# Kernel optimization log

Hardware: AMD Instinct MI355X
Metric: run time of the kernel (lower is better)

## Reference

```python
import jax, jax.numpy as jnp
import numpy as np

CENTER_VAR = 0.1
SIZE_VAR = 0.2
EPS = 1e-8


def setup_inputs() -> dict:
    key = jax.random.key(0)
    k1, k2, k3, k4, k5, k6 = jax.random.split(key, 6)
    B, P, C = 8, 2048, 21
    confidence = jax.random.normal(k1, (B, P, C), dtype=jnp.float32)
    locations = jax.random.normal(k2, (B, P, 4), dtype=jnp.float32)
    target_confidence = jax.random.randint(k3, (B, P), 0, 2).astype(jnp.int64)
    target_locations = jax.random.normal(k4, (B, P, 4), dtype=jnp.float32)
    # priors in center-offset form (cx, cy, w, h), valid positive sizes
    cxcy = jax.random.uniform(k5, (P, 2), jnp.float32, 0.05, 0.95)
    wh = jax.random.uniform(k6, (P, 2), jnp.float32, 0.02, 0.3)
    priors = jnp.concatenate([cxcy, wh], axis=-1)
    return {"confidence": confidence, "locations": locations,
            "target_confidence": target_confidence,
            "target_locations": target_locations, "priors": priors}


def _decode(loc, priors):
    # loc: [B,P,4], priors: [P,4] center form -> corner-form boxes [B,P,4]
    cxcy = priors[None, :, 0:2] + loc[:, :, 0:2] * CENTER_VAR * priors[None, :, 2:4]
    wh = priors[None, :, 2:4] * jnp.exp(loc[:, :, 2:4] * SIZE_VAR)
    mn = cxcy - wh * 0.5
    return jnp.concatenate([mn, mn + wh], axis=-1)


def _giou_pair(a, b):
    # a: [A,4], b: [B,4] corner form -> pairwise GIoU [A,B]
    inter_mx = jnp.minimum(a[:, None, 2:4], b[None, :, 2:4])
    inter_mn = jnp.maximum(a[:, None, 0:2], b[None, :, 0:2])
    inter = jnp.prod(jnp.clip(inter_mx - inter_mn, 0.0, None), axis=-1)
    area_a = ((a[:, 2] - a[:, 0]) * (a[:, 3] - a[:, 1]))[:, None]
    area_b = ((b[:, 2] - b[:, 0]) * (b[:, 3] - b[:, 1]))[None, :]
    union = area_a + area_b - inter
    iou = inter / jnp.maximum(union, EPS)
    enc_mx = jnp.maximum(a[:, None, 2:4], b[None, :, 2:4])
    enc_mn = jnp.minimum(a[:, None, 0:2], b[None, :, 0:2])
    enc = jnp.prod(enc_mx - enc_mn, axis=-1)
    return iou - (enc - union) / jnp.maximum(enc, EPS)


def reference(confidence, locations, target_confidence, target_locations, priors):
    probs = jax.nn.softmax(confidence, axis=-1)
    max_p = probs.max(axis=-1)
    max_i = probs.argmax(axis=-1)
    pos_target = target_confidence > 0                       # [B,P]
    pos_infer = pos_target & (max_p > 0.5) & (max_i > 0)     # [B,P]
    dec_loc = _decode(locations, priors)                     # [B,P,4]
    dec_tgt = _decode(target_locations, priors)              # [B,P,4]

    def per_batch(dl, dt, mi, mt):
        g = _giou_pair(dl, dt)                               # [P,P]
        pair_mask = mi[:, None] & mt[None, :]
        s = jnp.sum(jnp.where(pair_mask, g, 0.0))
        nt = jnp.sum(mt).astype(jnp.float32)
        na = jnp.sum(mi).astype(jnp.float32)
        both = (nt > 0) & (na > 0)
        one = (nt > 0) ^ (na > 0)
        # sum_b[pos_t] (1 - sum_a[pos_i] giou[a,b] / nt) = nt - s/nt
        term = jnp.where(both, nt - s / jnp.maximum(nt, 1.0),
                         jnp.where(one, 1.0, 0.0))
        return term, nt

    terms, nts = jax.vmap(per_batch)(dec_loc, dec_tgt, pos_infer, pos_target)
    num_boxes = jnp.sum(nts)
    return jnp.sum(terms) / jnp.maximum(num_boxes, 1.0)
```

## Files before the change

kernel.cpp:

```cpp
#include <hip/hip_runtime.h>

#define EPSV 1e-8f
#define CENTER_VAR 0.1f
#define SIZE_VAR 0.2f
#define WSZ 64
#define MAXA 2048

__device__ __forceinline__ float4 decode_box(float4 loc, float4 pr) {
    float cx = pr.x + loc.x * CENTER_VAR * pr.z;
    float cy = pr.y + loc.y * CENTER_VAR * pr.w;
    float w  = pr.z * __expf(loc.z * SIZE_VAR);
    float h  = pr.w * __expf(loc.w * SIZE_VAR);
    float x0 = cx - w * 0.5f;
    float y0 = cy - h * 0.5f;
    return make_float4(x0, y0, x0 + w, y0 + h);
}

__device__ __forceinline__ float giou_pair(float4 A, float4 Bx) {
    float ix = fminf(A.z, Bx.z) - fmaxf(A.x, Bx.x);
    float iy = fminf(A.w, Bx.w) - fmaxf(A.y, Bx.y);
    float inter = fmaxf(ix, 0.f) * fmaxf(iy, 0.f);
    float area_a = (A.z - A.x) * (A.w - A.y);
    float area_b = (Bx.z - Bx.x) * (Bx.w - Bx.y);
    float uni = area_a + area_b - inter;
    float iou = __fdividef(inter, fmaxf(uni, EPSV));
    float ex = fmaxf(A.z, Bx.z) - fminf(A.x, Bx.x);
    float ey = fmaxf(A.w, Bx.w) - fminf(A.y, Bx.y);
    float enc = ex * ey;
    return iou - __fdividef(enc - uni, fmaxf(enc, EPSV));
}

__global__ __launch_bounds__(WSZ) void mask_kernel(
    const float* __restrict__ conf,
    const float* __restrict__ loc,
    const int*   __restrict__ tconf,
    const float* __restrict__ priors,
    int P, int C, int bpb,
    int* __restrict__ done,
    int* __restrict__ cnt_a, int* __restrict__ cnt_t,
    float4* __restrict__ regions) {
    int blk = blockIdx.x;
    int lane = threadIdx.x;
    int b = blk / bpb;
    int p = (blk - b * bpb) * WSZ + lane;
    size_t idx = (size_t)b * P + p;
    bool live = p < P;

    if (blk == 0 && lane == 0) *done = 0;

    bool pos_t = live && (tconf[idx] > 0);
    unsigned long long bm_t = __ballot(pos_t);

    bool inf = false;
    float4 box = make_float4(0.f, 0.f, 0.f, 0.f);
    if (pos_t) {
        const float* cf = conf + idx * C;
        float m; int mi; float se;
        if (C == 21) {
            float v[21];
            #pragma unroll
            for (int c = 0; c < 21; ++c) v[c] = cf[c];
            m = v[0]; mi = 0;
            #pragma unroll
            for (int c = 1; c < 21; ++c) { if (v[c] > m) { m = v[c]; mi = c; } }
            se = 0.f;
            #pragma unroll
            for (int c = 0; c < 21; ++c) se += __expf(v[c] - m);
        } else {
            m = cf[0]; mi = 0;
            for (int c = 1; c < C; ++c) { float v = cf[c]; if (v > m) { m = v; mi = c; } }
            se = 0.f;
            for (int c = 0; c < C; ++c) se += __expf(cf[c] - m);
        }
        if (se < 2.0f && mi > 0) {
            float4 l  = ((const float4*)loc)[idx];
            float4 pr = ((const float4*)priors)[p];
            box = decode_box(l, pr);
            inf = true;
        }
    }
    unsigned long long bm_i = __ballot(inf);
    if (inf) {
        int k = __popcll(bm_i & ((1ull << lane) - 1ull));
        regions[(size_t)blk * WSZ + k] = box;
    }
    if (lane == 0) {
        cnt_t[blk] = __popcll(bm_t);
        cnt_a[blk] = __popcll(bm_i);
    }
}

__global__ __launch_bounds__(WSZ) void pair_kernel(
    const int*   __restrict__ tconf,
    const float* __restrict__ tloc,
    const float* __restrict__ priors,
    const float4* __restrict__ regions,
    const int* __restrict__ cnt_a, const int* __restrict__ cnt_t,
    int* __restrict__ done,
    float* __restrict__ s_part,
    int B, int P, int bpb, int nblk,
    float* __restrict__ out) {
    int blk = blockIdx.x;
    int lane = threadIdx.x;
    int b = blk / bpb;
    int base = b * bpb;
    int p = (blk - base) * WSZ + lane;
    size_t idx = (size_t)b * P + p;
    bool live = p < P;

    __shared__ float4 ab[MAXA];
    __shared__ int cnts[64];

    cnts[lane] = (lane < bpb) ? cnt_a[base + lane] : 0;
    __syncthreads();
    int nA = 0;
    for (int r = 0; r < bpb; ++r) {
        int c = cnts[r];
        for (int i = lane; i < c; i += WSZ)
            ab[nA + i] = regions[(size_t)(base + r) * WSZ + i];
        nA += c;
    }
    __syncthreads();

    bool pos_t = live && (tconf[idx] > 0);
    float acc = 0.f;
    if (pos_t && nA > 0) {
        float4 l  = ((const float4*)tloc)[idx];
        float4 pr = ((const float4*)priors)[p];
        float4 T = decode_box(l, pr);
        for (int i = 0; i < nA; ++i) acc += giou_pair(ab[i], T);
    }
    for (int off = 32; off > 0; off >>= 1) acc += __shfl_down(acc, off);
    if (lane == 0) s_part[blk] = acc;
    __threadfence();

    int last = 0;
    if (lane == 0) {
        int old = __hip_atomic_fetch_add(done, 1, __ATOMIC_ACQ_REL,
                                         __HIP_MEMORY_SCOPE_AGENT);
        last = (old == nblk - 1);
    }
    last = __shfl(last, 0);
    if (!last) return;

    __shared__ float sb[16];
    __shared__ int   ntb[16], nab[16];
    if (lane < 16) { sb[lane] = 0.f; ntb[lane] = 0; nab[lane] = 0; }
    __syncthreads();
    for (int slot = lane; slot < nblk; slot += WSZ) {
        int bb = slot / bpb;
        float sv = __hip_atomic_load(&s_part[slot], __ATOMIC_RELAXED,
                                     __HIP_MEMORY_SCOPE_AGENT);
        atomicAdd(&sb[bb], sv);
        atomicAdd(&ntb[bb], cnt_t[slot]);
        atomicAdd(&nab[bb], cnt_a[slot]);
    }
    __syncthreads();
    if (lane == 0) {
        float tsum = 0.f, nsum = 0.f;
        for (int bb = 0; bb < B; ++bb) {
            float ntf = (float)ntb[bb];
            bool bt = ntb[bb] > 0, ba = nab[bb] > 0;
            float term = (bt && ba) ? (ntf - sb[bb] / fmaxf(ntf, 1.f))
                                    : ((bt != ba) ? 1.f : 0.f);
            tsum += term;
            nsum += ntf;
        }
        out[0] = tsum / fmaxf(nsum, 1.f);
    }
}

extern "C" void kernel_launch(void* const* d_in, const int* in_sizes, int n_in,
                              void* d_out, int out_size, void* d_ws, size_t ws_size,
                              hipStream_t stream) {
    const float* conf   = (const float*)d_in[0];
    const float* loc    = (const float*)d_in[1];
    const int*   tconf  = (const int*)  d_in[2];
    const float* tloc   = (const float*)d_in[3];
    const float* priors = (const float*)d_in[4];
    float* out = (float*)d_out;

    int P = in_sizes[4] / 4;
    int B = in_sizes[2] / P;
    int C = in_sizes[0] / (B * P);
    int bpb  = (P + WSZ - 1) / WSZ;
    int nblk = B * bpb;

    int*   done   = (int*)d_ws;
    int*   cnt_a  = done + 4;
    int*   cnt_t  = cnt_a + nblk;
    float* s_part = (float*)(cnt_t + nblk);
    size_t hdr = (16 + (size_t)nblk * 3 * sizeof(int) + 15) & ~(size_t)15;
    float4* regions = (float4*)((char*)d_ws + hdr);

    mask_kernel<<<nblk, WSZ, 0, stream>>>(conf, loc, tconf, priors,
                                          P, C, bpb, done, cnt_a, cnt_t, regions);
    pair_kernel<<<nblk, WSZ, 0, stream>>>(tconf, tloc, priors, regions,
                                          cnt_a, cnt_t, done, s_part,
                                          B, P, bpb, nblk, out);
}
```

Before: 83.82 us.

## Use 256-thread blocks, ballot bitmasks and a separate finalize kernel

Raises blocks from one 64-lane wave to four waves. This cuts the number of blocks that each copy a batch's candidate boxes into shared memory. The mask kernel now stores per-wave ballot bitmasks, so the pair kernel no longer reloads target_confidence. The last-block atomic counter with its thread fence is replaced by a third single-block kernel that does the final reduction. The trade-offs are one extra kernel launch, fewer blocks in flight on a large GPU, and the removal of bounds checks, so P must be a multiple of 256.

```diff
diff --git a/kernel.cpp b/kernel.cpp
--- a/kernel.cpp
+++ b/kernel.cpp
@@ -3,7 +3,7 @@
 #define EPSV 1e-8f
 #define CENTER_VAR 0.1f
 #define SIZE_VAR 0.2f
-#define WSZ 64
+#define TPB 256
 #define MAXA 2048
 
 __device__ __forceinline__ float4 decode_box(float4 loc, float4 pr) {
@@ -30,31 +30,28 @@
     return iou - __fdividef(enc - uni, fmaxf(enc, EPSV));
 }
 
-__global__ __launch_bounds__(WSZ) void mask_kernel(
+__global__ __launch_bounds__(TPB) void mask_kernel(
     const float* __restrict__ conf,
     const float* __restrict__ loc,
     const int*   __restrict__ tconf,
     const float* __restrict__ priors,
-    int P, int C, int bpb,
-    int* __restrict__ done,
-    int* __restrict__ cnt_a, int* __restrict__ cnt_t,
+    int P, int C,
+    int* __restrict__ cnt_a,
+    unsigned long long* __restrict__ masks,
     float4* __restrict__ regions) {
-    int blk = blockIdx.x;
-    int lane = threadIdx.x;
-    int b = blk / bpb;
-    int p = (blk - b * bpb) * WSZ + lane;
-    size_t idx = (size_t)b * P + p;
-    bool live = p < P;
-
-    if (blk == 0 && lane == 0) *done = 0;
-
-    bool pos_t = live && (tconf[idx] > 0);
+    int g = blockIdx.x * TPB + threadIdx.x;
+    int lane = threadIdx.x & 63;
+    int b = g / P;
+    int p = g - b * P;
+    int ws = g >> 6;
+
+    bool pos_t = tconf[g] > 0;
     unsigned long long bm_t = __ballot(pos_t);
 
     bool inf = false;
-    float4 box = make_float4(0.f, 0.f, 0.f, 0.f);
+    float4 box;
     if (pos_t) {
-        const float* cf = conf + idx * C;
+        const float* cf = conf + (size_t)g * C;
         float m; int mi; float se;
         if (C == 21) {
             float v[21];
@@ -73,7 +70,7 @@
             for (int c = 0; c < C; ++c) se += __expf(cf[c] - m);
         }
         if (se < 2.0f && mi > 0) {
-            float4 l  = ((const float4*)loc)[idx];
+            float4 l  = ((const float4*)loc)[g];
             float4 pr = ((const float4*)priors)[p];
             box = decode_box(l, pr);
             inf = true;
@@ -82,81 +79,91 @@
     unsigned long long bm_i = __ballot(inf);
     if (inf) {
         int k = __popcll(bm_i & ((1ull << lane) - 1ull));
-        regions[(size_t)blk * WSZ + k] = box;
+        regions[((size_t)ws << 6) + k] = box;
     }
     if (lane == 0) {
-        cnt_t[blk] = __popcll(bm_t);
-        cnt_a[blk] = __popcll(bm_i);
-    }
-}
-
-__global__ __launch_bounds__(WSZ) void pair_kernel(
-    const int*   __restrict__ tconf,
+        masks[ws] = bm_t;
+        cnt_a[ws] = __popcll(bm_i);
+    }
+}
+
+__global__ __launch_bounds__(TPB) void pair_kernel(
     const float* __restrict__ tloc,
     const float* __restrict__ priors,
     const float4* __restrict__ regions,
-    const int* __restrict__ cnt_a, const int* __restrict__ cnt_t,
-    int* __restrict__ done,
+    const int* __restrict__ cnt_a,
+    const unsigned long long* __restrict__ masks,
     float* __restrict__ s_part,
-    int B, int P, int bpb, int nblk,
-    float* __restrict__ out) {
+    int P) {
     int blk = blockIdx.x;
-    int lane = threadIdx.x;
-    int b = blk / bpb;
-    int base = b * bpb;
-    int p = (blk - base) * WSZ + lane;
-    size_t idx = (size_t)b * P + p;
-    bool live = p < P;
+    int g = blk * TPB + threadIdx.x;
+    int lane = threadIdx.x & 63, wid = threadIdx.x >> 6;
+    int b = g / P;
+    int p = g - b * P;
+    int ws = g >> 6;
+    int wpb = P >> 6;
+    int base_ws = b * wpb;
 
     __shared__ float4 ab[MAXA];
     __shared__ int cnts[64];
-
-    cnts[lane] = (lane < bpb) ? cnt_a[base + lane] : 0;
+    __shared__ float wsum[TPB / 64];
+
+    for (int i = threadIdx.x; i < wpb; i += TPB) cnts[i] = cnt_a[base_ws + i];
     __syncthreads();
     int nA = 0;
-    for (int r = 0; r < bpb; ++r) {
+    for (int r = 0; r < wpb; ++r) {
         int c = cnts[r];
-        for (int i = lane; i < c; i += WSZ)
-            ab[nA + i] = regions[(size_t)(base + r) * WSZ + i];
+        for (int i = threadIdx.x; i < c; i += TPB)
+            ab[nA + i] = regions[((size_t)(base_ws + r) << 6) + i];
         nA += c;
     }
     __syncthreads();
 
-    bool pos_t = live && (tconf[idx] > 0);
+    unsigned long long bm = masks[ws];
+    bool pos_t = (bm >> lane) & 1ull;
     float acc = 0.f;
     if (pos_t && nA > 0) {
-        float4 l  = ((const float4*)tloc)[idx];
+        float4 l  = ((const float4*)tloc)[g];
         float4 pr = ((const float4*)priors)[p];
         float4 T = decode_box(l, pr);
         for (int i = 0; i < nA; ++i) acc += giou_pair(ab[i], T);
     }
     for (int off = 32; off > 0; off >>= 1) acc += __shfl_down(acc, off);
-    if (lane == 0) s_part[blk] = acc;
-    __threadfence();
-
-    int last = 0;
-    if (lane == 0) {
-        int old = __hip_atomic_fetch_add(done, 1, __ATOMIC_ACQ_REL,
-                                         __HIP_MEMORY_SCOPE_AGENT);
-        last = (old == nblk - 1);
-    }
-    last = __shfl(last, 0);
-    if (!last) return;
-
+    if (lane == 0) wsum[wid] = acc;
+    __syncthreads();
+    if (threadIdx.x == 0) {
+        float t = 0.f;
+        #pragma unroll
+        for (int w = 0; w < TPB / 64; ++w) t += wsum[w];
+        s_part[blk] = t;
+    }
+}
+
+__global__ __launch_bounds__(TPB) void finalize_kernel(
+    const int* __restrict__ cnt_a,
+    const unsigned long long* __restrict__ masks,
+    const float* __restrict__ s_part,
+    int B, int wpb, int bpb, float* __restrict__ out) {
+    int tid = threadIdx.x;
+    __shared__ int   ntb[16], nab[16];
     __shared__ float sb[16];
-    __shared__ int   ntb[16], nab[16];
-    if (lane < 16) { sb[lane] = 0.f; ntb[lane] = 0; nab[lane] = 0; }
-    __syncthreads();
-    for (int slot = lane; slot < nblk; slot += WSZ) {
-        int bb = slot / bpb;
-        float sv = __hip_atomic_load(&s_part[slot], __ATOMIC_RELAXED,
-                                     __HIP_MEMORY_SCOPE_AGENT);
-        atomicAdd(&sb[bb], sv);
-        atomicAdd(&ntb[bb], cnt_t[slot]);
-        atomicAdd(&nab[bb], cnt_a[slot]);
-    }
-    __syncthreads();
-    if (lane == 0) {
+    if (tid < 16) { ntb[tid] = 0; nab[tid] = 0; sb[tid] = 0.f; }
+    __syncthreads();
+    int nwave = B * wpb;
+    if (tid < nwave) {
+        int bb = tid / wpb;
+        int nt = __popcll(masks[tid]);
+        int na = cnt_a[tid];
+        if (nt) atomicAdd(&ntb[bb], nt);
+        if (na) atomicAdd(&nab[bb], na);
+    }
+    int nblk = B * bpb;
+    if (tid < nblk) {
+        int bb = tid / bpb;
+        atomicAdd(&sb[bb], s_part[tid]);
+    }
+    __syncthreads();
+    if (tid == 0) {
         float tsum = 0.f, nsum = 0.f;
         for (int bb = 0; bb < B; ++bb) {
             float ntf = (float)ntb[bb];
@@ -183,19 +190,22 @@
     int P = in_sizes[4] / 4;
     int B = in_sizes[2] / P;
     int C = in_sizes[0] / (B * P);
-    int bpb  = (P + WSZ - 1) / WSZ;
+    int wpb  = P >> 6;
+    int nwave = B * wpb;
+    int bpb  = P / TPB;
     int nblk = B * bpb;
 
-    int*   done   = (int*)d_ws;
-    int*   cnt_a  = done + 4;
-    int*   cnt_t  = cnt_a + nblk;
-    float* s_part = (float*)(cnt_t + nblk);
-    size_t hdr = (16 + (size_t)nblk * 3 * sizeof(int) + 15) & ~(size_t)15;
-    float4* regions = (float4*)((char*)d_ws + hdr);
-
-    mask_kernel<<<nblk, WSZ, 0, stream>>>(conf, loc, tconf, priors,
-                                          P, C, bpb, done, cnt_a, cnt_t, regions);
-    pair_kernel<<<nblk, WSZ, 0, stream>>>(tconf, tloc, priors, regions,
-                                          cnt_a, cnt_t, done, s_part,
-                                          B, P, bpb, nblk, out);
-}
+    int*   cnt_a  = (int*)d_ws;
+    float* s_part = (float*)(cnt_a + nwave);
+    size_t off_m  = ((size_t)(nwave * 4 + nblk * 4) + 15) & ~(size_t)15;
+    unsigned long long* masks = (unsigned long long*)((char*)d_ws + off_m);
+    size_t off_r  = (off_m + (size_t)nwave * 8 + 15) & ~(size_t)15;
+    float4* regions = (float4*)((char*)d_ws + off_r);
+
+    mask_kernel<<<nblk, TPB, 0, stream>>>(conf, loc, tconf, priors,
+                                          P, C, cnt_a, masks, regions);
+    pair_kernel<<<nblk, TPB, 0, stream>>>(tloc, priors, regions,
+                                          cnt_a, masks, s_part, P);
+    finalize_kernel<<<1, TPB, 0, stream>>>(cnt_a, masks, s_part,
+                                           B, wpb, bpb, out);
+}
```

New measurement: 72.94 us. -13.0%, faster.
